# Kernel optimization log

Measured on AMD Instinct MI355X. Metric: run time of the kernel, lower is better.

The kernel has to match this reference:

```python
import jax, jax.numpy as jnp
import numpy as np

B, N, DIM = 16, 1024, 768


def setup_inputs() -> dict:
    key = jax.random.key(0)
    ks = jax.random.split(key, 8)
    x = jax.random.normal(ks[0], (B, N, DIM), dtype=jnp.float32)
    y = jax.random.normal(ks[1], (B, N, DIM), dtype=jnp.float32)
    coords = jax.random.normal(ks[2], (N, N, 6), dtype=jnp.float32)
    # orthogonal init for U (as in torch init.orthogonal_)
    a = jax.random.normal(ks[3], (DIM, DIM), dtype=jnp.float32)
    q, r = jnp.linalg.qr(a)
    U = q * jnp.sign(jnp.diagonal(r))[None, :]
    S1 = jnp.ones((DIM,), dtype=jnp.float32)
    S2 = jnp.ones((DIM,), dtype=jnp.float32)
    gating = jnp.asarray(1.0, dtype=jnp.float32)
    temp = jnp.asarray(0.1, dtype=jnp.float32)
    pos_emb = jnp.zeros((N, 6, 1), dtype=jnp.float32)
    return {"x": x, "y": y, "coords": coords, "U": U, "S1": S1, "S2": S2,
            "gating": gating, "temp": temp, "pos_emb": pos_emb}


def reference(x, y, coords, U, S1, S2, gating, temp, pos_emb):
    dim = x.shape[-1]
    scale = dim ** (-0.5)
    # spectral decomposition: x @ U^T @ diag(S^2) @ U
    xu = x @ U.T                                   # [B,N,d]
    x1 = (xu * jnp.square(S1)) @ U                 # [B,N,d]
    x2 = (xu * jnp.square(S2)) @ U                 # [B,N,d]
    xs = jnp.stack([x1, x2], axis=1)               # [B,2,N,d]
    patch_score = jax.nn.softmax(
        jnp.einsum('bknd,bmd->bknm', xs, y) * scale, axis=-1)  # [B,2,N,M]
    pos = jnp.squeeze(coords @ pos_emb, -1)        # [N,M]
    pos_score = jax.nn.softmax(pos, axis=-1)[None, None]        # [1,1,N,M]
    g = jax.nn.sigmoid(gating)
    attn = (1.0 - g) * patch_score + g * pos_score  # [B,2,N,M]
    # entropy-routed gating
    entropy = jnp.sum(-attn * jnp.log(attn + 1e-8), axis=-1)    # [B,2,N]
    hmap = 2.0 - 2.0 * jax.nn.sigmoid(temp * jnp.transpose(entropy, (0, 2, 1)))  # [B,N,2]
    fgbg = hmap[..., 0] >= hmap[..., 1]
    route = jax.lax.stop_gradient(
        jnp.stack([fgbg, ~fgbg], axis=-1).astype(hmap.dtype))   # [B,N,2]
    heat_map = jnp.sum(hmap * route, axis=-1, keepdims=True)    # [B,N,1]
    attn_c = jnp.sum(attn * jnp.transpose(route, (0, 2, 1))[..., None], axis=1)  # [B,N,M]
    out = attn_c @ y                               # [B,N,d]
    return (out, heat_map)
```

## Files before the change

kernel.cpp:

```cpp
#include <hip/hip_runtime.h>
#include <hip/hip_bf16.h>

#define DEV __device__ __forceinline__

typedef unsigned short u16;
typedef short short8 __attribute__((ext_vector_type(8)));
typedef float f32x4 __attribute__((ext_vector_type(4)));

static const int BB = 16;
static const int NN = 1024;
static const int DD = 768;

DEV u16 f2bf(float f) {
    unsigned u = __builtin_bit_cast(unsigned, f);
    unsigned r = u + 0x7fffu + ((u >> 16) & 1u);
    return (u16)(r >> 16);
}
DEV float h2f(u16 u) { return (float)__builtin_bit_cast(_Float16, u); }
DEV u16 f2h(float f) { return __builtin_bit_cast(u16, (_Float16)f); }

DEV short8 ldf8_bf(const float* p) {
    float4 f0 = *(const float4*)p;
    float4 f1 = *(const float4*)(p + 4);
    short8 r;
    r[0] = (short)f2bf(f0.x); r[1] = (short)f2bf(f0.y);
    r[2] = (short)f2bf(f0.z); r[3] = (short)f2bf(f0.w);
    r[4] = (short)f2bf(f1.x); r[5] = (short)f2bf(f1.y);
    r[6] = (short)f2bf(f1.z); r[7] = (short)f2bf(f1.w);
    return r;
}

DEV void gl_lds16(const u16* g, u16* l) {
    __builtin_amdgcn_global_load_lds(
        (const __attribute__((address_space(1))) unsigned int*)g,
        (__attribute__((address_space(3))) unsigned int*)l, 16, 0, 0);
}

template<int OM>
__global__ __launch_bounds__(256) void gemm128(
    const u16* __restrict__ Ag, const u16* __restrict__ Bg, void* __restrict__ Cg,
    int K, int N, int zmod,
    long sA0, long sA1, long sB0, long sB1, long sC0, long sC1,
    float scale)
{
    __shared__ u16 As[128 * 32];
    __shared__ u16 Bs[128 * 32];

    int z = blockIdx.z;
    const u16* A = Ag + (long)(z % zmod) * sA0 + (long)(z / zmod) * sA1;
    const u16* B = Bg + (long)(z % zmod) * sB0 + (long)(z / zmod) * sB1;
    u16*   Cu = (u16*)Cg   + (long)(z % zmod) * sC0 + (long)(z / zmod) * sC1;
    float* Cf = (float*)Cg + (long)(z % zmod) * sC0 + (long)(z / zmod) * sC1;

    int tid  = threadIdx.x;
    int lane = tid & 63, wave = tid >> 6;
    int wm = wave & 1, wn = wave >> 1;
    int lr = lane & 15, quad = lane >> 4;

    long m0 = (long)blockIdx.x * 128;
    long n0 = (long)blockIdx.y * 128;

    int p0 = tid, p1 = tid + 256;
    int ar0 = p0 >> 2, aq0 = (p0 & 3) ^ ((ar0 >> 1) & 3);
    int ar1 = p1 >> 2, aq1 = (p1 & 3) ^ ((ar1 >> 1) & 3);
    const u16* a0p = A + (m0 + ar0) * (long)K + aq0 * 8;
    const u16* a1p = A + (m0 + ar1) * (long)K + aq1 * 8;
    const u16* b0p = B + (n0 + ar0) * (long)K + aq0 * 8;
    const u16* b1p = B + (n0 + ar1) * (long)K + aq1 * 8;
    u16* lA0 = As + p0 * 8;  u16* lA1 = As + p1 * 8;
    u16* lB0 = Bs + p0 * 8;  u16* lB1 = Bs + p1 * 8;

    int aoff[4], boff[4];
#pragma unroll
    for (int t = 0; t < 4; t++) {
        int ra = wm * 64 + t * 16 + lr;
        int rb = wn * 64 + t * 16 + lr;
        aoff[t] = ra * 32 + ((quad ^ ((ra >> 1) & 3)) * 8);
        boff[t] = rb * 32 + ((quad ^ ((rb >> 1) & 3)) * 8);
    }

    f32x4 acc[4][4] = {};

    for (int k0 = 0; k0 < K; k0 += 32) {
        gl_lds16(a0p + k0, lA0);
        gl_lds16(a1p + k0, lA1);
        gl_lds16(b0p + k0, lB0);
        gl_lds16(b1p + k0, lB1);
        __syncthreads();

        short8 af[4], bfr[4];
#pragma unroll
        for (int t = 0; t < 4; t++) af[t]  = *(const short8*)(As + aoff[t]);
#pragma unroll
        for (int t = 0; t < 4; t++) bfr[t] = *(const short8*)(Bs + boff[t]);
#pragma unroll
        for (int ti = 0; ti < 4; ti++)
#pragma unroll
            for (int tj = 0; tj < 4; tj++)
                acc[ti][tj] = __builtin_amdgcn_mfma_f32_16x16x32_bf16(
                    af[ti], bfr[tj], acc[ti][tj], 0, 0, 0);
        __syncthreads();
    }

    long crow = m0 + wm * 64 + quad * 4;
    long ccol = n0 + wn * 64 + lr;
#pragma unroll
    for (int ti = 0; ti < 4; ti++)
#pragma unroll
        for (int tj = 0; tj < 4; tj++)
#pragma unroll
            for (int r = 0; r < 4; r++) {
                long row = crow + ti * 16 + r;
                long col = ccol + tj * 16;
                float v = acc[ti][tj][r] * scale;
                long idx = row * (long)N + col;
                if constexpr (OM == 0)      Cu[idx] = f2bf(v);
                else if constexpr (OM == 1) Cu[idx] = f2h(v);
                else                        Cf[idx] = v;
            }
}

__global__ __launch_bounds__(256) void k_prep_u(
    const float* __restrict__ U, const float* __restrict__ S1,
    const float* __restrict__ S2, u16* __restrict__ Ub,
    u16* __restrict__ VT1, u16* __restrict__ VT2)
{
    __shared__ float tile[32][33];
    int i0 = blockIdx.x * 32, j0 = blockIdx.y * 32;
#pragma unroll
    for (int r = 0; r < 32; r += 8) {
        int i = i0 + threadIdx.y + r, j = j0 + threadIdx.x;
        float v = U[(long)i * DD + j];
        tile[threadIdx.y + r][threadIdx.x] = v;
        Ub[(long)i * DD + j] = f2bf(v);
    }
    __syncthreads();
    float s1v = S1[i0 + threadIdx.x];
    float s2v = S2[i0 + threadIdx.x];
    s1v *= s1v; s2v *= s2v;
#pragma unroll
    for (int r = 0; r < 32; r += 8) {
        int j = j0 + threadIdx.y + r, i = i0 + threadIdx.x;
        float v = tile[threadIdx.x][threadIdx.y + r];
        VT1[(long)j * DD + i] = f2bf(s1v * v);
        VT2[(long)j * DD + i] = f2bf(s2v * v);
    }
}

__global__ __launch_bounds__(256) void k_conv_x(
    const float* __restrict__ x, u16* __restrict__ xb)
{
    long i = ((long)blockIdx.x * 256 + threadIdx.x) * 8;
    *(short8*)(xb + i) = ldf8_bf(x + i);
}

__global__ __launch_bounds__(256) void k_conv_y(
    const float* __restrict__ y, u16* __restrict__ yb, u16* __restrict__ yT)
{
    __shared__ float tile[32][33];
    int b = blockIdx.z;
    int d0 = blockIdx.x * 32, m0 = blockIdx.y * 32;
    const float* ybase = y + (long)b * NN * DD;
#pragma unroll
    for (int r = 0; r < 32; r += 8) {
        int m = m0 + threadIdx.y + r, d = d0 + threadIdx.x;
        float v = ybase[(long)m * DD + d];
        tile[threadIdx.y + r][threadIdx.x] = v;
        yb[(long)b * NN * DD + (long)m * DD + d] = f2bf(v);
    }
    __syncthreads();
#pragma unroll
    for (int r = 0; r < 32; r += 8) {
        int d = d0 + threadIdx.y + r, m = m0 + threadIdx.x;
        yT[(long)b * DD * NN + (long)d * NN + m] = f2bf(tile[threadIdx.x][threadIdx.y + r]);
    }
}

DEV float wave_red_max(float v) {
#pragma unroll
    for (int o = 32; o; o >>= 1) v = fmaxf(v, __shfl_xor(v, o));
    return v;
}
DEV float wave_red_sum(float v) {
#pragma unroll
    for (int o = 32; o; o >>= 1) v += __shfl_xor(v, o);
    return v;
}
DEV float block_red_max(float v, float* sh) {
    v = wave_red_max(v);
    if ((threadIdx.x & 63) == 0) sh[threadIdx.x >> 6] = v;
    __syncthreads();
    v = fmaxf(fmaxf(sh[0], sh[1]), fmaxf(sh[2], sh[3]));
    __syncthreads();
    return v;
}
DEV float block_red_sum(float v, float* sh) {
    v = wave_red_sum(v);
    if ((threadIdx.x & 63) == 0) sh[threadIdx.x >> 6] = v;
    __syncthreads();
    v = (sh[0] + sh[1]) + (sh[2] + sh[3]);
    __syncthreads();
    return v;
}

__global__ __launch_bounds__(256) void k_pos(
    const float* __restrict__ coords, const float* __restrict__ pe,
    float* __restrict__ P)
{
    __shared__ float sh[4];
    int n = blockIdx.x, t = threadIdx.x;
    float p6[6];
#pragma unroll
    for (int c = 0; c < 6; c++) p6[c] = pe[n * 6 + c];
    float v[4];
#pragma unroll
    for (int i = 0; i < 4; i++) {
        const float* cp = coords + ((long)n * NN + t * 4 + i) * 6;
        v[i] = p6[0]*cp[0] + p6[1]*cp[1] + p6[2]*cp[2] + p6[3]*cp[3] + p6[4]*cp[4] + p6[5]*cp[5];
    }
    float mx = block_red_max(fmaxf(fmaxf(v[0], v[1]), fmaxf(v[2], v[3])), sh);
    float e[4], s = 0.f;
#pragma unroll
    for (int i = 0; i < 4; i++) { e[i] = expf(v[i] - mx); s += e[i]; }
    float Z = block_red_sum(s, sh);
    float inv = 1.f / Z;
    float4 o; o.x = e[0]*inv; o.y = e[1]*inv; o.z = e[2]*inv; o.w = e[3]*inv;
    *(float4*)(P + ((long)n << 10) + t * 4) = o;
}

__global__ __launch_bounds__(256) void k_route(
    u16* __restrict__ S, const float* __restrict__ P,
    const float* __restrict__ gating, const float* __restrict__ temp,
    float* __restrict__ heat)
{
    __shared__ float sh[4];
    int bn = blockIdx.x;
    int b = bn >> 10, n = bn & 1023, t = threadIdx.x;
    u16* s1p = S + ((long)(b * 2) << 20) + ((long)n << 10) + t * 4;
    u16* s2p = s1p + (1L << 20);
    const float* pp = P + ((long)n << 10) + t * 4;

    ushort4 r1 = *(const ushort4*)s1p;
    ushort4 r2 = *(const ushort4*)s2p;
    float4 pv = *(const float4*)pp;
    float s1[4] = { h2f(r1.x), h2f(r1.y), h2f(r1.z), h2f(r1.w) };
    float s2[4] = { h2f(r2.x), h2f(r2.y), h2f(r2.z), h2f(r2.w) };
    float p4[4] = { pv.x, pv.y, pv.z, pv.w };

    float mx1 = block_red_max(fmaxf(fmaxf(s1[0], s1[1]), fmaxf(s1[2], s1[3])), sh);
    float mx2 = block_red_max(fmaxf(fmaxf(s2[0], s2[1]), fmaxf(s2[2], s2[3])), sh);

    float e1[4], e2[4], z1 = 0.f, z2 = 0.f;
#pragma unroll
    for (int i = 0; i < 4; i++) {
        e1[i] = expf(s1[i] - mx1); z1 += e1[i];
        e2[i] = expf(s2[i] - mx2); z2 += e2[i];
    }
    float Z1 = block_red_sum(z1, sh);
    float Z2 = block_red_sum(z2, sh);

    float g = 1.f / (1.f + expf(-gating[0]));
    float c1 = (1.f - g) / Z1, c2 = (1.f - g) / Z2;

    float a1[4], a2[4], hh1 = 0.f, hh2 = 0.f;
#pragma unroll
    for (int i = 0; i < 4; i++) {
        a1[i] = e1[i] * c1 + g * p4[i];
        a2[i] = e2[i] * c2 + g * p4[i];
        hh1 -= a1[i] * logf(a1[i] + 1e-8f);
        hh2 -= a2[i] * logf(a2[i] + 1e-8f);
    }
    float H1 = block_red_sum(hh1, sh);
    float H2 = block_red_sum(hh2, sh);

    float tv = temp[0];
    float hm0 = 2.f - 2.f / (1.f + expf(-tv * H1));
    float hm1 = 2.f - 2.f / (1.f + expf(-tv * H2));
    int ks = (hm0 >= hm1) ? 0 : 1;
    if (t == 0) heat[bn] = ks ? hm1 : hm0;

    ushort4 w;
    w.x = f2bf(ks ? a2[0] : a1[0]);
    w.y = f2bf(ks ? a2[1] : a1[1]);
    w.z = f2bf(ks ? a2[2] : a1[2]);
    w.w = f2bf(ks ? a2[3] : a1[3]);
    *(ushort4*)s1p = w;
}

extern "C" void kernel_launch(void* const* d_in, const int* in_sizes, int n_in,
                              void* d_out, int out_size, void* d_ws, size_t ws_size,
                              hipStream_t stream)
{
    (void)in_sizes; (void)n_in; (void)out_size; (void)ws_size;
    const float* x      = (const float*)d_in[0];
    const float* y      = (const float*)d_in[1];
    const float* coords = (const float*)d_in[2];
    const float* U      = (const float*)d_in[3];
    const float* S1     = (const float*)d_in[4];
    const float* S2     = (const float*)d_in[5];
    const float* gating = (const float*)d_in[6];
    const float* temp   = (const float*)d_in[7];
    const float* pose   = (const float*)d_in[8];

    float* out  = (float*)d_out;
    float* heat = out + (long)BB * NN * DD;

    char* w = (char*)d_ws;
    u16* Ub  = (u16*)w;  w += (long)DD * DD * 2;
    u16* VT  = (u16*)w;  w += (long)2 * DD * DD * 2;
    u16* xb  = (u16*)w;  w += (long)BB * NN * DD * 2;
    u16* x12 = (u16*)w;  w += (long)2 * BB * NN * DD * 2;
    u16* yb  = (u16*)w;  w += (long)BB * NN * DD * 2;
    u16* yT  = (u16*)w;  w += (long)BB * DD * NN * 2;
    u16* S   = (u16*)w;  w += (long)BB * 2 * NN * NN * 2;
    float* P = (float*)w;
    u16* xu  = S;

    const long MBN = (long)BB * NN * DD;
    const long BND = (long)NN * DD;
    const long SPL = (long)NN * NN;

    k_prep_u<<<dim3(24, 24), dim3(32, 8), 0, stream>>>(U, S1, S2, Ub, VT, VT + (long)DD * DD);
    k_conv_x<<<dim3(MBN / 2048), dim3(256), 0, stream>>>(x, xb);
    k_conv_y<<<dim3(DD / 32, NN / 32, BB), dim3(32, 8), 0, stream>>>(y, yb, yT);
    k_pos<<<dim3(NN), dim3(256), 0, stream>>>(coords, pose, P);

    gemm128<0><<<dim3(BB * NN / 128, DD / 128, 1), dim3(256), 0, stream>>>(
        xb, Ub, xu, DD, DD, 1,
        0L, 0L, 0L, 0L, 0L, 0L, 1.0f);

    gemm128<0><<<dim3(BB * NN / 128, DD / 128, 2), dim3(256), 0, stream>>>(
        xu, VT, x12, DD, DD, 2,
        0L, 0L, (long)DD * DD, 0L, MBN, 0L, 1.0f);

    gemm128<1><<<dim3(NN / 128, NN / 128, BB * 2), dim3(256), 0, stream>>>(
        x12, yb, S, DD, NN, 2,
        MBN, BND, 0L, BND, SPL, 2 * SPL, 0.036084391824351615f);

    k_route<<<dim3(BB * NN), dim3(256), 0, stream>>>(S, P, gating, temp, heat);

    gemm128<2><<<dim3(NN / 128, DD / 128, BB), dim3(256), 0, stream>>>(
        S, yT, out, NN, DD, 1,
        0L, 2 * SPL, 0L, BND, 0L, BND, 1.0f);
}
```

Baseline: 431.3 us.

## Precompute U^T diag(S^2) U weights and deepen GEMM K-tile to 64

Reassociates the spectral product so the two small DxD matrices W = U^T diag(S^2) U are formed once. x is then multiplied directly by W, replacing the large x@U^T GEMM over B*N rows with a DxD GEMM. Separately, the shared GEMM kernel now loads a K-slice of 64 per barrier instead of 32, with a wider XOR swizzle, halving the number of sync iterations. The trade-offs are extra bf16 rounding in the fused W product and doubled LDS use per block, which may lower occupancy.

```diff
diff --git a/kernel.cpp b/kernel.cpp
--- a/kernel.cpp
+++ b/kernel.cpp
@@ -43,8 +43,8 @@
     long sA0, long sA1, long sB0, long sB1, long sC0, long sC1,
     float scale)
 {
-    __shared__ u16 As[128 * 32];
-    __shared__ u16 Bs[128 * 32];
+    __shared__ u16 As[128 * 64];
+    __shared__ u16 Bs[128 * 64];
 
     int z = blockIdx.z;
     const u16* A = Ag + (long)(z % zmod) * sA0 + (long)(z / zmod) * sA1;
@@ -60,45 +60,54 @@
     long m0 = (long)blockIdx.x * 128;
     long n0 = (long)blockIdx.y * 128;
 
-    int p0 = tid, p1 = tid + 256;
-    int ar0 = p0 >> 2, aq0 = (p0 & 3) ^ ((ar0 >> 1) & 3);
-    int ar1 = p1 >> 2, aq1 = (p1 & 3) ^ ((ar1 >> 1) & 3);
-    const u16* a0p = A + (m0 + ar0) * (long)K + aq0 * 8;
-    const u16* a1p = A + (m0 + ar1) * (long)K + aq1 * 8;
-    const u16* b0p = B + (n0 + ar0) * (long)K + aq0 * 8;
-    const u16* b1p = B + (n0 + ar1) * (long)K + aq1 * 8;
-    u16* lA0 = As + p0 * 8;  u16* lA1 = As + p1 * 8;
-    u16* lB0 = Bs + p0 * 8;  u16* lB1 = Bs + p1 * 8;
-
-    int aoff[4], boff[4];
+    long aOfs[4], bOfs[4];
+    u16 *lA[4], *lB[4];
+#pragma unroll
+    for (int i = 0; i < 4; i++) {
+        int p = tid + i * 256;
+        int row = p >> 3, qs = p & 7;
+        int q = qs ^ (row & 7);
+        aOfs[i] = (m0 + row) * (long)K + q * 8;
+        bOfs[i] = (n0 + row) * (long)K + q * 8;
+        lA[i] = As + p * 8;
+        lB[i] = Bs + p * 8;
+    }
+
+    int aoff[4][2], boff[4][2];
 #pragma unroll
     for (int t = 0; t < 4; t++) {
         int ra = wm * 64 + t * 16 + lr;
         int rb = wn * 64 + t * 16 + lr;
-        aoff[t] = ra * 32 + ((quad ^ ((ra >> 1) & 3)) * 8);
-        boff[t] = rb * 32 + ((quad ^ ((rb >> 1) & 3)) * 8);
+#pragma unroll
+        for (int h = 0; h < 2; h++) {
+            aoff[t][h] = ra * 64 + (((h * 4 + quad) ^ (ra & 7)) * 8);
+            boff[t][h] = rb * 64 + (((h * 4 + quad) ^ (rb & 7)) * 8);
+        }
     }
 
     f32x4 acc[4][4] = {};
 
-    for (int k0 = 0; k0 < K; k0 += 32) {
-        gl_lds16(a0p + k0, lA0);
-        gl_lds16(a1p + k0, lA1);
-        gl_lds16(b0p + k0, lB0);
-        gl_lds16(b1p + k0, lB1);
+    for (int k0 = 0; k0 < K; k0 += 64) {
+#pragma unroll
+        for (int i = 0; i < 4; i++) gl_lds16(A + aOfs[i] + k0, lA[i]);
+#pragma unroll
+        for (int i = 0; i < 4; i++) gl_lds16(B + bOfs[i] + k0, lB[i]);
         __syncthreads();
 
-        short8 af[4], bfr[4];
-#pragma unroll
-        for (int t = 0; t < 4; t++) af[t]  = *(const short8*)(As + aoff[t]);
-#pragma unroll
-        for (int t = 0; t < 4; t++) bfr[t] = *(const short8*)(Bs + boff[t]);
-#pragma unroll
-        for (int ti = 0; ti < 4; ti++)
-#pragma unroll
-            for (int tj = 0; tj < 4; tj++)
-                acc[ti][tj] = __builtin_amdgcn_mfma_f32_16x16x32_bf16(
-                    af[ti], bfr[tj], acc[ti][tj], 0, 0, 0);
+#pragma unroll
+        for (int h = 0; h < 2; h++) {
+            short8 af[4], bfr[4];
+#pragma unroll
+            for (int t = 0; t < 4; t++) af[t]  = *(const short8*)(As + aoff[t][h]);
+#pragma unroll
+            for (int t = 0; t < 4; t++) bfr[t] = *(const short8*)(Bs + boff[t][h]);
+#pragma unroll
+            for (int ti = 0; ti < 4; ti++)
+#pragma unroll
+                for (int tj = 0; tj < 4; tj++)
+                    acc[ti][tj] = __builtin_amdgcn_mfma_f32_16x16x32_bf16(
+                        af[ti], bfr[tj], acc[ti][tj], 0, 0, 0);
+        }
         __syncthreads();
     }
 
@@ -122,7 +131,7 @@
 
 __global__ __launch_bounds__(256) void k_prep_u(
     const float* __restrict__ U, const float* __restrict__ S1,
-    const float* __restrict__ S2, u16* __restrict__ Ub,
+    const float* __restrict__ S2, u16* __restrict__ UTb,
     u16* __restrict__ VT1, u16* __restrict__ VT2)
 {
     __shared__ float tile[32][33];
@@ -130,9 +139,7 @@
 #pragma unroll
     for (int r = 0; r < 32; r += 8) {
         int i = i0 + threadIdx.y + r, j = j0 + threadIdx.x;
-        float v = U[(long)i * DD + j];
-        tile[threadIdx.y + r][threadIdx.x] = v;
-        Ub[(long)i * DD + j] = f2bf(v);
+        tile[threadIdx.y + r][threadIdx.x] = U[(long)i * DD + j];
     }
     __syncthreads();
     float s1v = S1[i0 + threadIdx.x];
@@ -142,6 +149,7 @@
     for (int r = 0; r < 32; r += 8) {
         int j = j0 + threadIdx.y + r, i = i0 + threadIdx.x;
         float v = tile[threadIdx.x][threadIdx.y + r];
+        UTb[(long)j * DD + i] = f2bf(v);
         VT1[(long)j * DD + i] = f2bf(s1v * v);
         VT2[(long)j * DD + i] = f2bf(s2v * v);
     }
@@ -306,32 +314,33 @@
     float* heat = out + (long)BB * NN * DD;
 
     char* w = (char*)d_ws;
-    u16* Ub  = (u16*)w;  w += (long)DD * DD * 2;
+    u16* UTb = (u16*)w;  w += (long)DD * DD * 2;
     u16* VT  = (u16*)w;  w += (long)2 * DD * DD * 2;
+    u16* W2  = (u16*)w;  w += (long)2 * DD * DD * 2;
     u16* xb  = (u16*)w;  w += (long)BB * NN * DD * 2;
     u16* x12 = (u16*)w;  w += (long)2 * BB * NN * DD * 2;
     u16* yb  = (u16*)w;  w += (long)BB * NN * DD * 2;
     u16* yT  = (u16*)w;  w += (long)BB * DD * NN * 2;
     u16* S   = (u16*)w;  w += (long)BB * 2 * NN * NN * 2;
     float* P = (float*)w;
-    u16* xu  = S;
 
     const long MBN = (long)BB * NN * DD;
     const long BND = (long)NN * DD;
     const long SPL = (long)NN * NN;
-
-    k_prep_u<<<dim3(24, 24), dim3(32, 8), 0, stream>>>(U, S1, S2, Ub, VT, VT + (long)DD * DD);
+    const long DSQ = (long)DD * DD;
+
+    k_prep_u<<<dim3(24, 24), dim3(32, 8), 0, stream>>>(U, S1, S2, UTb, VT, VT + DSQ);
     k_conv_x<<<dim3(MBN / 2048), dim3(256), 0, stream>>>(x, xb);
     k_conv_y<<<dim3(DD / 32, NN / 32, BB), dim3(32, 8), 0, stream>>>(y, yb, yT);
     k_pos<<<dim3(NN), dim3(256), 0, stream>>>(coords, pose, P);
 
-    gemm128<0><<<dim3(BB * NN / 128, DD / 128, 1), dim3(256), 0, stream>>>(
-        xb, Ub, xu, DD, DD, 1,
-        0L, 0L, 0L, 0L, 0L, 0L, 1.0f);
+    gemm128<0><<<dim3(DD / 128, DD / 128, 2), dim3(256), 0, stream>>>(
+        UTb, VT, W2, DD, DD, 2,
+        0L, 0L, DSQ, 0L, DSQ, 0L, 1.0f);
 
     gemm128<0><<<dim3(BB * NN / 128, DD / 128, 2), dim3(256), 0, stream>>>(
-        xu, VT, x12, DD, DD, 2,
-        0L, 0L, (long)DD * DD, 0L, MBN, 0L, 1.0f);
+        xb, W2, x12, DD, DD, 2,
+        0L, 0L, DSQ, 0L, MBN, 0L, 1.0f);
 
     gemm128<1><<<dim3(NN / 128, NN / 128, BB * 2), dim3(256), 0, stream>>>(
         x12, yb, S, DD, NN, 2,
```

Result: faster. 400.2 us (-7.2%).
